# Optimization experiments

Measured on AMD Instinct MI355X. Metric: run time of the kernel, lower is better.

Reference implementation:

```python
import jax, jax.numpy as jnp
import numpy as np
from functools import partial

IN_CH, OUT_CH, HID = 16, 20, 256
B, T = 64, 4096
LEAKY_SLOPE = 0.01  # torch LeakyReLU default


def _lstm_layer(x_seq, Wih, Whh, bih, bhh):
    """Single-layer LSTM over a full sequence.

    x_seq: (T, B, Din). Weights use PyTorch layout: W (4H, Din/H), gate order i,f,g,o.
    Returns hidden states (T, B, H).
    """
    H = Whh.shape[1]
    Tlen, Bsz = x_seq.shape[0], x_seq.shape[1]
    # Precompute input contributions for all timesteps in one GEMM.
    xw = jnp.einsum('tbd,gd->tbg', x_seq, Wih) + (bih + bhh)  # (T, B, 4H)

    def step(carry, xw_t):
        h, c = carry
        gates = xw_t + h @ Whh.T  # (B, 4H)
        i, f, g, o = jnp.split(gates, 4, axis=-1)
        i = jax.nn.sigmoid(i)
        f = jax.nn.sigmoid(f)
        g = jnp.tanh(g)
        o = jax.nn.sigmoid(o)
        c = f * c + i * g
        h = o * jnp.tanh(c)
        return (h, c), h

    h0 = jnp.zeros((Bsz, H), dtype=x_seq.dtype)
    c0 = jnp.zeros((Bsz, H), dtype=x_seq.dtype)
    _, hs = jax.lax.scan(step, (h0, c0), xw)
    return hs  # (T, B, H)


def setup_inputs() -> dict:
    key = jax.random.key(0)
    ks = jax.random.split(key, 12)
    s = 1.0 / np.sqrt(HID)  # torch nn.LSTM init scale
    return {
        'x': jax.random.normal(ks[0], (B, IN_CH, T), dtype=jnp.float32),
        'Wih0': jax.random.normal(ks[1], (4 * HID, IN_CH), dtype=jnp.float32) * s,
        'Whh0': jax.random.normal(ks[2], (4 * HID, HID), dtype=jnp.float32) * s,
        'bih0': jax.random.normal(ks[3], (4 * HID,), dtype=jnp.float32) * s,
        'bhh0': jax.random.normal(ks[4], (4 * HID,), dtype=jnp.float32) * s,
        'Wih1': jax.random.normal(ks[5], (4 * HID, HID), dtype=jnp.float32) * s,
        'Whh1': jax.random.normal(ks[6], (4 * HID, HID), dtype=jnp.float32) * s,
        'bih1': jax.random.normal(ks[7], (4 * HID,), dtype=jnp.float32) * s,
        'bhh1': jax.random.normal(ks[8], (4 * HID,), dtype=jnp.float32) * s,
        'Whead': jax.random.normal(ks[9], (OUT_CH, HID), dtype=jnp.float32) * s,
        'bhead': jax.random.normal(ks[10], (OUT_CH,), dtype=jnp.float32) * s,
    }


def reference(x, Wih0, Whh0, bih0, bhh0, Wih1, Whh1, bih1, bhh1, Whead, bhead):
    # x: (B, C_in, T) -> time-major (T, B, C_in)
    xs = jnp.transpose(x, (2, 0, 1))
    h1 = _lstm_layer(xs, Wih0, Whh0, bih0, bhh0)   # (T, B, H)
    h2 = _lstm_layer(h1, Wih1, Whh1, bih1, bhh1)   # (T, B, H)
    # Head: LeakyReLU then Linear, applied per timestep (vectorized).
    a = jnp.where(h2 >= 0, h2, LEAKY_SLOPE * h2)
    y = jnp.einsum('tbh,oh->tbo', a, Whead) + bhead  # (T, B, OUT)
    return jnp.transpose(y, (1, 2, 0))  # (B, C_out, T)
```

## Files before the change

### kernel.cpp

```cpp
#include <hip/hip_runtime.h>
#include <hip/hip_fp16.h>
#include <stdint.h>


#define T_SEQ 4096
#define NB    64
#define HID   256
#define G4    1024
#define INCH  16
#define OC    20

typedef _Float16 h2v   __attribute__((ext_vector_type(2)));
typedef _Float16 f16x8 __attribute__((ext_vector_type(8)));
typedef float    f32x4 __attribute__((ext_vector_type(4)));

__device__ __forceinline__ float fdot2(uint32_t a, uint32_t b, float c) {
  return __builtin_amdgcn_fdot2(__builtin_bit_cast(h2v, a),
                                __builtin_bit_cast(h2v, b), c, false);
}
__device__ __forceinline__ float sigf(float x) {
  x = fminf(fmaxf(x, -30.f), 30.f);
  return 1.f / (1.f + __expf(-x));
}
__device__ __forceinline__ float tanhf_fast(float x) {
  x = fminf(fmaxf(x, -15.f), 15.f);
  float e = __expf(-2.f * x);
  return (1.f - e) / (1.f + e);
}

#define PIN(x) asm volatile("" : "+v"(x))

struct SmemR {
  __half w[256 * 264];
  uint32_t hbuf[2][144];
  float bsum[1024];
  union {
    uint32_t xb[512 * 8];
    struct {
      __half abuf[2][320];
      __half whd[20 * 264];
      float  bh[20];
    } h1;
  } u;
};
struct SmemG {
  __half a[128 * 40];
  __half b[64 * 40];
};
union Smem { SmemR r; SmemG g; };

struct Params {
  const float* x;
  const __half *wh0, *wh1, *wi0, *wi1, *whd;
  const float  *bs0, *bs1, *bhd;
  float *h0s, *c0s, *h1s, *c1s;
  __half* h1w; const __half* h1r;
  float* xww;  const float* xwr;
  float* y;
  int L, Tc, nch;
};

template <int LAYER>
__device__ void role_rec(SmemR& S, int ch, const Params& P, int b) {
  if (ch < 0 || ch >= P.nch) return;
  const int tid   = threadIdx.x;
  const int slice = tid & 3;
  const int rg    = tid >> 2;
  const int Tc    = P.Tc;
  const __half* whh = (LAYER == 0) ? P.wh0 : P.wh1;

  for (int i = tid; i < 8192; i += 512) {
    int R = i >> 5, oct = i & 31;
    *(uint4*)&S.w[R * 264 + oct * 8] =
        *((const uint4*)(whh + (768 + R) * 256) + oct);
  }
  {
    const float* bs = (LAYER == 0) ? P.bs0 : P.bs1;
    for (int i = tid; i < 1024; i += 512) S.bsum[i] = bs[i];
  }
  const int t0 = ch * Tc;
  if (LAYER == 0) {
    for (int i = tid; i < Tc * 8; i += 512) {
      int dp = i / Tc, tt = i - dp * Tc;
      float v0 = P.x[(b * INCH + 2 * dp) * T_SEQ + t0 + tt];
      float v1 = P.x[(b * INCH + 2 * dp + 1) * T_SEQ + t0 + tt];
      uint32_t pv = (uint32_t)__half_as_ushort(__float2half(v0)) |
                    ((uint32_t)__half_as_ushort(__float2half(v1)) << 16);
      S.u.xb[tt * 8 + dp] = pv;
    }
  } else {
    for (int i = tid; i < OC * 256; i += 512) {
      int o = i >> 8, k = i & 255;
      S.u.h1.whd[o * 264 + k] = P.whd[i];
    }
    if (tid < OC) S.u.h1.bh[tid] = P.bhd[tid];
  }

  uint32_t wr[6][32];
#pragma unroll
  for (int j = 0; j < 6; j++) {
    const uint4* p = (const uint4*)(whh + (rg + 128 * j) * 256 + slice * 64);
#pragma unroll
    for (int q = 0; q < 8; q++) {
      uint4 v = p[q];
      wr[j][4 * q] = v.x; wr[j][4 * q + 1] = v.y;
      wr[j][4 * q + 2] = v.z; wr[j][4 * q + 3] = v.w;
    }
  }
#pragma unroll
  for (int j = 0; j < 6; j++)
#pragma unroll
    for (int q = 0; q < 32; q++) PIN(wr[j][q]);

  uint32_t wx[8][2];
  if (LAYER == 0) {
#pragma unroll
    for (int j = 0; j < 8; j++) {
      const uint32_t* p = (const uint32_t*)(P.wi0 + (rg + 128 * j) * INCH + slice * 4);
      wx[j][0] = p[0]; wx[j][1] = p[1];
    }
#pragma unroll
    for (int j = 0; j < 8; j++) { PIN(wx[j][0]); PIN(wx[j][1]); }
  }

  float* hs = (LAYER == 0) ? P.h0s : P.h1s;
  float* cs = (LAYER == 0) ? P.c0s : P.c1s;
  float hA = 0.f, hB = 0.f, cA = 0.f, cB = 0.f;
  if (slice == 0) {
    if (ch != 0) {
      hA = hs[b * 256 + rg];       cA = cs[b * 256 + rg];
      hB = hs[b * 256 + rg + 128]; cB = cs[b * 256 + rg + 128];
    }
    __half* hb = (__half*)S.hbuf[0];
    hb[(rg >> 6) * 72 + (rg & 63)] = __float2half(hA);
    hb[(2 + (rg >> 6)) * 72 + (rg & 63)] = __float2half(hB);
  }
  float xwpre[8];
  if (LAYER == 1 && slice == 0) {
#pragma unroll
    for (int j = 0; j < 8; j++)
      xwpre[j] = P.xwr[(0 * NB + b) * G4 + rg + 128 * j];
  }
  __syncthreads();

  for (int tt = 0; tt < Tc; ++tt) {
    const __half* hb = (const __half*)S.hbuf[tt & 1];
    float acc[8];
#pragma unroll
    for (int j = 0; j < 8; j++) acc[j] = 0.f;

#pragma unroll
    for (int hf = 0; hf < 2; ++hf) {
      uint32_t hh[16];
      const uint4* hp = (const uint4*)(hb + slice * 72 + hf * 32);
#pragma unroll
      for (int q = 0; q < 4; q++) {
        uint4 v = hp[q];
        hh[4 * q] = v.x; hh[4 * q + 1] = v.y; hh[4 * q + 2] = v.z; hh[4 * q + 3] = v.w;
      }
#pragma unroll
      for (int j = 0; j < 6; j++) {
        float a = acc[j];
#pragma unroll
        for (int q = 0; q < 16; q++) a = fdot2(wr[j][hf * 16 + q], hh[q], a);
        acc[j] = a;
      }
#pragma unroll
      for (int j = 6; j < 8; j++) {
        const uint4* wp =
            (const uint4*)&S.w[((j - 6) * 128 + rg) * 264 + slice * 64 + hf * 32];
        float a = acc[j];
#pragma unroll
        for (int q = 0; q < 4; q++) {
          uint4 v = wp[q];
          a = fdot2(v.x, hh[4 * q], a);
          a = fdot2(v.y, hh[4 * q + 1], a);
          a = fdot2(v.z, hh[4 * q + 2], a);
          a = fdot2(v.w, hh[4 * q + 3], a);
        }
        acc[j] = a;
      }
    }
    if (LAYER == 0) {
      uint32_t xv0 = S.u.xb[tt * 8 + 2 * slice];
      uint32_t xv1 = S.u.xb[tt * 8 + 2 * slice + 1];
#pragma unroll
      for (int j = 0; j < 8; j++) {
        acc[j] = fdot2(wx[j][0], xv0, acc[j]);
        acc[j] = fdot2(wx[j][1], xv1, acc[j]);
      }
    }
#pragma unroll
    for (int j = 0; j < 8; j++) {
      acc[j] += __shfl_xor(acc[j], 1);
      acc[j] += __shfl_xor(acc[j], 2);
    }

    if (slice == 0) {
      float g[8];
#pragma unroll
      for (int j = 0; j < 8; j++) g[j] = acc[j] + S.bsum[rg + 128 * j];
      if (LAYER == 1) {
#pragma unroll
        for (int j = 0; j < 8; j++) g[j] += xwpre[j];
        if (tt + 1 < Tc) {
#pragma unroll
          for (int j = 0; j < 8; j++)
            xwpre[j] = P.xwr[((tt + 1) * NB + b) * G4 + rg + 128 * j];
        }
      }
      float iA = sigf(g[0]), iB = sigf(g[1]);
      float fA = sigf(g[2]), fB = sigf(g[3]);
      float gA = tanhf_fast(g[4]), gB = tanhf_fast(g[5]);
      float oA = sigf(g[6]), oB = sigf(g[7]);
      cA = fA * cA + iA * gA;
      cB = fB * cB + iB * gB;
      hA = oA * tanhf_fast(cA);
      hB = oB * tanhf_fast(cB);
      __half hA16 = __float2half(hA), hB16 = __float2half(hB);
      __half* hw = (__half*)S.hbuf[(tt + 1) & 1];
      hw[(rg >> 6) * 72 + (rg & 63)] = hA16;
      hw[(2 + (rg >> 6)) * 72 + (rg & 63)] = hB16;
      if (LAYER == 0) {
        __half* dst = P.h1w + (size_t)(tt * NB + b) * 256;
        dst[rg] = hA16;
        dst[rg + 128] = hB16;
      } else {
        float aA = hA > 0.f ? hA : 0.01f * hA;
        float aB = hB > 0.f ? hB : 0.01f * hB;
        __half* ab = S.u.h1.abuf[tt & 1];
        ab[(rg >> 5) * 40 + (rg & 31)] = __float2half(aA);
        ab[(4 + (rg >> 5)) * 40 + (rg & 31)] = __float2half(aB);
      }
    }
    __syncthreads();

    if (LAYER == 1 && tid < OC * 8) {
      int o = tid >> 3, ks = tid & 7;
      const uint4* wp = (const uint4*)&S.u.h1.whd[o * 264 + ks * 32];
      const uint4* ap = (const uint4*)&S.u.h1.abuf[tt & 1][ks * 40];
      float a = 0.f;
#pragma unroll
      for (int q = 0; q < 4; q++) {
        uint4 w4 = wp[q];
        uint4 a4 = ap[q];
        a = fdot2(w4.x, a4.x, a);
        a = fdot2(w4.y, a4.y, a);
        a = fdot2(w4.z, a4.z, a);
        a = fdot2(w4.w, a4.w, a);
      }
      a += __shfl_xor(a, 1);
      a += __shfl_xor(a, 2);
      a += __shfl_xor(a, 4);
      if (ks == 0) P.y[(b * OC + o) * T_SEQ + t0 + tt] = a + S.u.h1.bh[o];
    }
  }
  if (slice == 0) {
    hs[b * 256 + rg] = hA;        cs[b * 256 + rg] = cA;
    hs[b * 256 + rg + 128] = hB;  cs[b * 256 + rg + 128] = cB;
  }
}

__device__ void role_gemm(SmemG& S, int chG, const Params& P) {
  if (chG < 0 || chG >= P.nch) return;
  const int bid = blockIdx.x - 128;
  const int nt = bid & 15, mt = bid >> 4;
  const int tb0 = mt * 128, g0 = nt * 64;
  const int tid = threadIdx.x, lane = tid & 63, w = tid >> 6;
  const int wm = w & 3, wn = w >> 2;

  f32x4 cacc[2][2] = {};
  for (int kk = 0; kk < 256; kk += 32) {
    __syncthreads();
    {
      int row = tid >> 2, q = tid & 3;
      const uint4* src = (const uint4*)(P.h1r + (tb0 + row) * 256 + kk + q * 8);
      *(uint4*)&S.a[row * 40 + q * 8] = *src;
    }
    if (tid < 256) {
      int row = tid >> 2, q = tid & 3;
      const uint4* src = (const uint4*)(P.wi1 + (g0 + row) * 256 + kk + q * 8);
      *(uint4*)&S.b[row * 40 + q * 8] = *src;
    }
    __syncthreads();
    f16x8 af[2], bf[2];
#pragma unroll
    for (int mi = 0; mi < 2; mi++)
      af[mi] = *(const f16x8*)&S.a[(wm * 32 + mi * 16 + (lane & 15)) * 40 + (lane >> 4) * 8];
#pragma unroll
    for (int ni = 0; ni < 2; ni++)
      bf[ni] = *(const f16x8*)&S.b[(wn * 32 + ni * 16 + (lane & 15)) * 40 + (lane >> 4) * 8];
#pragma unroll
    for (int mi = 0; mi < 2; mi++)
#pragma unroll
      for (int ni = 0; ni < 2; ni++)
        cacc[mi][ni] = __builtin_amdgcn_mfma_f32_16x16x32_f16(af[mi], bf[ni], cacc[mi][ni], 0, 0, 0);
  }
#pragma unroll
  for (int mi = 0; mi < 2; mi++)
#pragma unroll
    for (int ni = 0; ni < 2; ni++) {
      int m = wm * 32 + mi * 16 + (lane >> 4) * 4;
      int n = g0 + wn * 32 + ni * 16 + (lane & 15);
#pragma unroll
      for (int r = 0; r < 4; r++)
        P.xww[(size_t)(tb0 + m + r) * G4 + n] = cacc[mi][ni][r];
    }
}

__global__ __launch_bounds__(512)
__attribute__((amdgpu_waves_per_eu(2, 2)))
void fused_kernel(Params P) {
  __shared__ Smem S;
  int bid = blockIdx.x;
  if (bid < 64)        role_rec<0>(S.r, P.L, P, bid);
  else if (bid < 128)  role_rec<1>(S.r, P.L - 2, P, bid - 64);
  else                 role_gemm(S.g, P.L - 1, P);
}

__global__ void prep_kernel(const float* Wih0, const float* Whh0,
                            const float* bih0, const float* bhh0,
                            const float* Wih1, const float* Whh1,
                            const float* bih1, const float* bhh1,
                            const float* Whead, const float* bhead,
                            __half* wh0, __half* wh1, __half* wi1, __half* wi0,
                            __half* whd, float* bs0, float* bs1, float* bhd) {
  int i = blockIdx.x * blockDim.x + threadIdx.x;
  if (i < G4 * HID) {
    wh0[i] = __float2half(Whh0[i]);
    wh1[i] = __float2half(Whh1[i]);
    wi1[i] = __float2half(Wih1[i]);
  }
  if (i < G4 * INCH) wi0[i] = __float2half(Wih0[i]);
  if (i < OC * HID)  whd[i] = __float2half(Whead[i]);
  if (i < G4) { bs0[i] = bih0[i] + bhh0[i]; bs1[i] = bih1[i] + bhh1[i]; }
  if (i < OC) bhd[i] = bhead[i];
}

extern "C" void kernel_launch(void* const* d_in, const int* in_sizes, int n_in,
                              void* d_out, int out_size, void* d_ws, size_t ws_size,
                              hipStream_t stream) {
  const float* x     = (const float*)d_in[0];
  const float* Wih0  = (const float*)d_in[1];
  const float* Whh0  = (const float*)d_in[2];
  const float* bih0  = (const float*)d_in[3];
  const float* bhh0  = (const float*)d_in[4];
  const float* Wih1  = (const float*)d_in[5];
  const float* Whh1  = (const float*)d_in[6];
  const float* bih1  = (const float*)d_in[7];
  const float* bhh1  = (const float*)d_in[8];
  const float* Whead = (const float*)d_in[9];
  const float* bhead = (const float*)d_in[10];
  float* y = (float*)d_out;

  char* ws = (char*)d_ws;
  size_t cur = 0;
  auto alloc = [&](size_t sz) -> char* {
    char* p = ws + cur;
    cur = (cur + sz + 255) & ~(size_t)255;
    return p;
  };
  __half* wh0 = (__half*)alloc(G4 * HID * 2);
  __half* wh1 = (__half*)alloc(G4 * HID * 2);
  __half* wi1 = (__half*)alloc(G4 * HID * 2);
  __half* wi0 = (__half*)alloc(G4 * INCH * 2);
  __half* whd = (__half*)alloc(OC * HID * 2);
  float* bs0 = (float*)alloc(G4 * 4);
  float* bs1 = (float*)alloc(G4 * 4);
  float* bhd = (float*)alloc(OC * 4);
  float* h0s = (float*)alloc(NB * HID * 4);
  float* c0s = (float*)alloc(NB * HID * 4);
  float* h1s = (float*)alloc(NB * HID * 4);
  float* c1s = (float*)alloc(NB * HID * 4);
  size_t fixed = cur;

  int Tc = 512;
  while (Tc > 64) {
    size_t need = fixed + 2 * ((size_t)Tc * NB * HID * 2 + 512) +
                  2 * ((size_t)Tc * NB * G4 * 4 + 512);
    if (need <= ws_size) break;
    Tc >>= 1;
  }
  __half* h1buf[2];
  float* xwbuf[2];
  h1buf[0] = (__half*)alloc((size_t)Tc * NB * HID * 2);
  h1buf[1] = (__half*)alloc((size_t)Tc * NB * HID * 2);
  xwbuf[0] = (float*)alloc((size_t)Tc * NB * G4 * 4);
  xwbuf[1] = (float*)alloc((size_t)Tc * NB * G4 * 4);

  const int nch = T_SEQ / Tc;

  prep_kernel<<<(G4 * HID + 255) / 256, 256, 0, stream>>>(
      Wih0, Whh0, bih0, bhh0, Wih1, Whh1, bih1, bhh1, Whead, bhead,
      wh0, wh1, wi1, wi0, whd, bs0, bs1, bhd);

  const int ngemm = Tc * 8;
  for (int L = 0; L < nch + 2; ++L) {
    Params P;
    P.x = x;
    P.wh0 = wh0; P.wh1 = wh1; P.wi0 = wi0; P.wi1 = wi1; P.whd = whd;
    P.bs0 = bs0; P.bs1 = bs1; P.bhd = bhd;
    P.h0s = h0s; P.c0s = c0s; P.h1s = h1s; P.c1s = c1s;
    P.h1w = h1buf[L & 1];
    P.h1r = h1buf[(L + 1) & 1];
    P.xww = xwbuf[(L + 1) & 1];
    P.xwr = xwbuf[L & 1];
    P.y = y;
    P.L = L; P.Tc = Tc; P.nch = nch;
    fused_kernel<<<128 + ngemm, 512, 0, stream>>>(P);
  }
}
```

Before: 10.92 ms.

## Split LSTM gate activation across two lanes per quad using DPP reductions

Replaces the shfl_xor quad reduction with DPP quad-permute adds, so all four lanes hold the full sums. The gate nonlinearity and cell update are then split between two lanes per quad (one per hidden channel) instead of serialising both channels on slice 0. Biases move from shared memory into registers. The layer-1 input-projection loads are issued at the top of each step, and the layer-0 global store of h is deferred by one step, to take latency off the serial critical path. This adds register pressure and relies on the DPP control encodings being correct.

New measurement: 9.867 ms. 1.11x faster.

```diff
diff --git a/kernel.cpp b/kernel.cpp
--- a/kernel.cpp
+++ b/kernel.cpp
@@ -27,13 +27,19 @@
   float e = __expf(-2.f * x);
   return (1.f - e) / (1.f + e);
 }
+__device__ __forceinline__ float quad_sum(float a) {
+  a += __int_as_float(
+      __builtin_amdgcn_update_dpp(0, __float_as_int(a), 0xB1, 0xF, 0xF, true));
+  a += __int_as_float(
+      __builtin_amdgcn_update_dpp(0, __float_as_int(a), 0x4E, 0xF, 0xF, true));
+  return a;
+}
 
 #define PIN(x) asm volatile("" : "+v"(x))
 
 struct SmemR {
   __half w[256 * 264];
   uint32_t hbuf[2][144];
-  float bsum[1024];
   union {
     uint32_t xb[512 * 8];
     struct {
@@ -74,10 +80,6 @@
     *(uint4*)&S.w[R * 264 + oct * 8] =
         *((const uint4*)(whh + (768 + R) * 256) + oct);
   }
-  {
-    const float* bs = (LAYER == 0) ? P.bs0 : P.bs1;
-    for (int i = tid; i < 1024; i += 512) S.bsum[i] = bs[i];
-  }
   const int t0 = ch * Tc;
   if (LAYER == 0) {
     for (int i = tid; i < Tc * 8; i += 512) {
@@ -123,28 +125,37 @@
     for (int j = 0; j < 8; j++) { PIN(wx[j][0]); PIN(wx[j][1]); }
   }
 
+  const bool own = (slice < 2);
+  const int chn = rg + ((slice & 1) << 7);
   float* hs = (LAYER == 0) ? P.h0s : P.h1s;
   float* cs = (LAYER == 0) ? P.c0s : P.c1s;
-  float hA = 0.f, hB = 0.f, cA = 0.f, cB = 0.f;
-  if (slice == 0) {
-    if (ch != 0) {
-      hA = hs[b * 256 + rg];       cA = cs[b * 256 + rg];
-      hB = hs[b * 256 + rg + 128]; cB = cs[b * 256 + rg + 128];
-    }
-    __half* hb = (__half*)S.hbuf[0];
-    hb[(rg >> 6) * 72 + (rg & 63)] = __float2half(hA);
-    hb[(2 + (rg >> 6)) * 72 + (rg & 63)] = __float2half(hB);
-  }
-  float xwpre[8];
-  if (LAYER == 1 && slice == 0) {
-#pragma unroll
-    for (int j = 0; j < 8; j++)
-      xwpre[j] = P.xwr[(0 * NB + b) * G4 + rg + 128 * j];
-  }
+  float bs4[4] = {0.f, 0.f, 0.f, 0.f};
+  float hO = 0.f, cO = 0.f;
+  if (own) {
+    const float* bsg = (LAYER == 0) ? P.bs0 : P.bs1;
+#pragma unroll
+    for (int k = 0; k < 4; k++) bs4[k] = bsg[chn + 256 * k];
+    if (ch != 0) { hO = hs[b * 256 + chn]; cO = cs[b * 256 + chn]; }
+    ((__half*)S.hbuf[0])[(chn >> 6) * 72 + (chn & 63)] = __float2half(hO);
+  }
+  const float* xp = (LAYER == 1 && own) ? (P.xwr + (size_t)b * G4 + chn)
+                                        : (const float*)nullptr;
   __syncthreads();
 
+  const __half* hbA = (const __half*)S.hbuf[0] + slice * 72;
+  const __half* hbB = (const __half*)S.hbuf[1] + slice * 72;
+  __half hprev = __float2half(0.f);
+  float xwv[4] = {0.f, 0.f, 0.f, 0.f};
+
   for (int tt = 0; tt < Tc; ++tt) {
-    const __half* hb = (const __half*)S.hbuf[tt & 1];
+    if (LAYER == 0 && own && tt > 0)
+      P.h1w[(size_t)((tt - 1) * NB + b) * 256 + chn] = hprev;
+    if (LAYER == 1 && own) {
+      const float* q = xp + (size_t)tt * (NB * G4);
+      xwv[0] = q[0]; xwv[1] = q[256]; xwv[2] = q[512]; xwv[3] = q[768];
+    }
+
+    const __half* hb = (tt & 1) ? hbB : hbA;
     float acc[8];
 #pragma unroll
     for (int j = 0; j < 8; j++) acc[j] = 0.f;
@@ -152,7 +163,7 @@
 #pragma unroll
     for (int hf = 0; hf < 2; ++hf) {
       uint32_t hh[16];
-      const uint4* hp = (const uint4*)(hb + slice * 72 + hf * 32);
+      const uint4* hp = (const uint4*)(hb + hf * 32);
 #pragma unroll
       for (int q = 0; q < 4; q++) {
         uint4 v = hp[q];
@@ -191,46 +202,26 @@
       }
     }
 #pragma unroll
-    for (int j = 0; j < 8; j++) {
-      acc[j] += __shfl_xor(acc[j], 1);
-      acc[j] += __shfl_xor(acc[j], 2);
-    }
-
-    if (slice == 0) {
-      float g[8];
-#pragma unroll
-      for (int j = 0; j < 8; j++) g[j] = acc[j] + S.bsum[rg + 128 * j];
-      if (LAYER == 1) {
-#pragma unroll
-        for (int j = 0; j < 8; j++) g[j] += xwpre[j];
-        if (tt + 1 < Tc) {
-#pragma unroll
-          for (int j = 0; j < 8; j++)
-            xwpre[j] = P.xwr[((tt + 1) * NB + b) * G4 + rg + 128 * j];
-        }
-      }
-      float iA = sigf(g[0]), iB = sigf(g[1]);
-      float fA = sigf(g[2]), fB = sigf(g[3]);
-      float gA = tanhf_fast(g[4]), gB = tanhf_fast(g[5]);
-      float oA = sigf(g[6]), oB = sigf(g[7]);
-      cA = fA * cA + iA * gA;
-      cB = fB * cB + iB * gB;
-      hA = oA * tanhf_fast(cA);
-      hB = oB * tanhf_fast(cB);
-      __half hA16 = __float2half(hA), hB16 = __float2half(hB);
-      __half* hw = (__half*)S.hbuf[(tt + 1) & 1];
-      hw[(rg >> 6) * 72 + (rg & 63)] = hA16;
-      hw[(2 + (rg >> 6)) * 72 + (rg & 63)] = hB16;
+    for (int j = 0; j < 8; j++) acc[j] = quad_sum(acc[j]);
+
+    if (own) {
+      const int o = slice & 1;
+      float gi = acc[0 + o] + bs4[0];
+      float gf = acc[2 + o] + bs4[1];
+      float gg = acc[4 + o] + bs4[2];
+      float go = acc[6 + o] + bs4[3];
+      if (LAYER == 1) { gi += xwv[0]; gf += xwv[1]; gg += xwv[2]; go += xwv[3]; }
+      float iv = sigf(gi), fv = sigf(gf);
+      float gv = tanhf_fast(gg), ov = sigf(go);
+      cO = fv * cO + iv * gv;
+      hO = ov * tanhf_fast(cO);
+      __half h16 = __float2half(hO);
+      ((__half*)S.hbuf[(tt + 1) & 1])[(chn >> 6) * 72 + (chn & 63)] = h16;
       if (LAYER == 0) {
-        __half* dst = P.h1w + (size_t)(tt * NB + b) * 256;
-        dst[rg] = hA16;
-        dst[rg + 128] = hB16;
+        hprev = h16;
       } else {
-        float aA = hA > 0.f ? hA : 0.01f * hA;
-        float aB = hB > 0.f ? hB : 0.01f * hB;
-        __half* ab = S.u.h1.abuf[tt & 1];
-        ab[(rg >> 5) * 40 + (rg & 31)] = __float2half(aA);
-        ab[(4 + (rg >> 5)) * 40 + (rg & 31)] = __float2half(aB);
+        float av = hO > 0.f ? hO : 0.01f * hO;
+        S.u.h1.abuf[tt & 1][(chn >> 5) * 40 + (chn & 31)] = __float2half(av);
       }
     }
     __syncthreads();
@@ -255,9 +246,11 @@
       if (ks == 0) P.y[(b * OC + o) * T_SEQ + t0 + tt] = a + S.u.h1.bh[o];
     }
   }
-  if (slice == 0) {
-    hs[b * 256 + rg] = hA;        cs[b * 256 + rg] = cA;
-    hs[b * 256 + rg + 128] = hB;  cs[b * 256 + rg + 128] = cB;
+  if (own) {
+    if (LAYER == 0)
+      P.h1w[(size_t)((Tc - 1) * NB + b) * 256 + chn] = hprev;
+    hs[b * 256 + chn] = hO;
+    cs[b * 256 + chn] = cO;
   }
 }
 
```
